# Kernel tuning notes

Measured on AMD Instinct MI355X. Metric: run time of the kernel, lower is better.

The kernel has to match this reference:

```python
import jax, jax.numpy as jnp
import numpy as np

EMBED_DIM = 64  # scale factor dim (matches head dim)


def setup_inputs() -> dict:
    key0 = jax.random.key(0)
    kq, kk, kv = jax.random.split(key0, 3)
    shape = (2, 16, 2048, 64)  # [B, H, S, D]
    return {
        "query": jax.random.normal(kq, shape, dtype=jnp.float32),
        "key": jax.random.normal(kk, shape, dtype=jnp.float32),
        "value": jax.random.normal(kv, shape, dtype=jnp.float32),
    }


def reference(query, key, value):
    # qk = Q K^T / sqrt(embed_dim); softmax over last dim; @ V
    inv_scale = jnp.sqrt(jnp.asarray(EMBED_DIM, dtype=query.dtype))
    scores = jnp.einsum("bhqd,bhkd->bhqk", query, key) / inv_scale
    probs = jax.nn.softmax(scores, axis=-1)
    # dropout_p=0.0 -> identity (eval semantics)
    return jnp.einsum("bhqk,bhkd->bhqd", probs, value)
```

## Files before the change

### kernel.cpp

```cpp
#include <hip/hip_runtime.h>
#include <hip/hip_bf16.h>

#define S_LEN 2048
#define DDIM  64
#define NT    (S_LEN / 64)
#define SCALE  0.125f
#define SCALE2 0.18033688f
#define NELEM  4194304
#define NQROW  65536

typedef __attribute__((ext_vector_type(8))) short short8;
typedef __attribute__((ext_vector_type(4))) short short4v;
typedef __attribute__((ext_vector_type(4))) float floatx4;

__device__ __forceinline__ short f2bf(float f) {
    union { float f; unsigned u; } v; v.f = f;
    return (short)((v.u + 0x7fffu + ((v.u >> 16) & 1u)) >> 16);
}

__device__ __forceinline__ unsigned pk2bf(float a, float b) {
#if __has_builtin(__builtin_amdgcn_cvt_pk_bf16_f32)
    auto r = __builtin_amdgcn_cvt_pk_bf16_f32(a, b);
    union { decltype(r) v; unsigned u; } c; c.v = r; return c.u;
#else
    union { float f; unsigned u; } x, y; x.f = a; y.f = b;
    unsigned lo = (x.u + 0x7fffu + ((x.u >> 16) & 1u)) >> 16;
    unsigned hi = (y.u + 0x7fffu + ((y.u >> 16) & 1u)) & 0xffff0000u;
    return lo | hi;
#endif
}

__device__ __forceinline__ float fexp2(float x) {
#if __has_builtin(__builtin_amdgcn_exp2f)
    return __builtin_amdgcn_exp2f(x);
#else
    return exp2f(x);
#endif
}

__device__ __forceinline__ void dma16(const void* g, void* l) {
    __builtin_amdgcn_global_load_lds(
        (const __attribute__((address_space(1))) void*)g,
        (__attribute__((address_space(3))) void*)l, 16, 0, 0);
}

__global__ __launch_bounds__(256) void prep_kv(const float* __restrict__ K,
                                               const float* __restrict__ V,
                                               short* __restrict__ Kb,
                                               short* __restrict__ Vt) {
    __shared__ short T[64 * 68];
    const int bh = blockIdx.x & 31;
    const int st = blockIdx.x >> 5;
    const int t  = threadIdx.x;
    const size_t tile_off = (size_t)bh * (S_LEN * DDIM) + (size_t)st * (64 * DDIM);

    {
        const float* src = K + tile_off + t * 16;
        short* dst = Kb + tile_off + t * 16;
        #pragma unroll
        for (int h = 0; h < 2; ++h) {
            float4 a = *(const float4*)(src + h * 8);
            float4 b = *(const float4*)(src + h * 8 + 4);
            uint4 o;
            o.x = pk2bf(a.x, a.y); o.y = pk2bf(a.z, a.w);
            o.z = pk2bf(b.x, b.y); o.w = pk2bf(b.z, b.w);
            *(uint4*)(dst + h * 8) = o;
        }
    }

    const float* src = V + tile_off;
    const int skey = t >> 2, scol = (t & 3) * 4;
    #pragma unroll
    for (int i = 0; i < 4; ++i) {
        const int c = scol + i * 16;
        float4 v = *(const float4*)(src + (size_t)skey * 64 + c);
        uint2 o; o.x = pk2bf(v.x, v.y); o.y = pk2bf(v.z, v.w);
        *(uint2*)&T[skey * 68 + c] = o;
    }
    __syncthreads();
    const int d = t >> 2, cb = (t & 3) * 16;
    short8 o0, o1;
    #pragma unroll
    for (int j = 0; j < 8; ++j) {
        o0[j] = T[(cb + j) * 68 + d];
        o1[j] = T[(cb + 8 + j) * 68 + d];
    }
    short* dst = Vt + (size_t)bh * (DDIM * S_LEN) + (size_t)d * S_LEN + st * 64 + cb;
    *(short8*)dst       = o0;
    *(short8*)(dst + 8) = o1;
}

template <int NSPLIT>
__global__ __launch_bounds__(256) void attn_sm(
    const float* __restrict__ Q, const short* __restrict__ Kb,
    const short* __restrict__ Vt, float* __restrict__ O,
    float* __restrict__ numer, float* __restrict__ denom)
{
    __shared__ short Ks[2][64 * 64];
    __shared__ short Vs[64 * 64];
    __shared__ short Pl[4][32 * 64];

    constexpr int NIT = NT / NSPLIT;

    const int tid  = threadIdx.x;
    const int wave = tid >> 6;
    const int lane = tid & 63;
    const int l16  = lane & 15;
    const int quad = lane >> 4;
    const int x7   = l16 & 7;

    const int bh = blockIdx.x & 31;
    const int rest = blockIdx.x >> 5;
    const int qt = rest & 15;
    const int ks = rest >> 4;
    const size_t base = (size_t)bh * (S_LEN * DDIM);

    const int ci0 = tid,        r0 = ci0 >> 3, c0 = (ci0 & 7) ^ (r0 & 7);
    const int ci1 = 256 + tid,  r1 = ci1 >> 3, c1 = (ci1 & 7) ^ (r1 & 7);
    const size_t koff = (size_t)ks * NIT * (64 * 64);
    const size_t voff = (size_t)ks * NIT * 64;
    const short* pK0 = Kb + base + koff + r0 * 64 + c0 * 8;
    const short* pK1 = Kb + base + koff + r1 * 64 + c1 * 8;
    const short* pV0 = Vt + base + voff + (size_t)r0 * S_LEN + c0 * 8;
    const short* pV1 = Vt + base + voff + (size_t)r1 * S_LEN + c1 * 8;

    dma16(pK0, &Ks[0][ci0 * 8]);
    dma16(pK1, &Ks[0][ci1 * 8]);

    short8 qf[2][2];
    #pragma unroll
    for (int nq = 0; nq < 2; ++nq) {
        const float* qp = Q + base + (size_t)(qt * 128 + wave * 32 + nq * 16 + l16) * 64 + quad * 8;
        #pragma unroll
        for (int kt = 0; kt < 2; ++kt) {
            float4 a = *(const float4*)(qp + kt * 32);
            float4 b = *(const float4*)(qp + kt * 32 + 4);
            union { unsigned u[4]; short8 s; } qc;
            qc.u[0] = pk2bf(a.x * SCALE2, a.y * SCALE2);
            qc.u[1] = pk2bf(a.z * SCALE2, a.w * SCALE2);
            qc.u[2] = pk2bf(b.x * SCALE2, b.y * SCALE2);
            qc.u[3] = pk2bf(b.z * SCALE2, b.w * SCALE2);
            qf[nq][kt] = qc.s;
        }
    }

    floatx4 oacc[2][4];
    float rs[2];
    #pragma unroll
    for (int mt = 0; mt < 2; ++mt) {
        #pragma unroll
        for (int dt = 0; dt < 4; ++dt) oacc[mt][dt] = (floatx4){0.f,0.f,0.f,0.f};
        rs[mt] = 0.f;
    }

    short* Pw = &Pl[wave][0];

    for (int kb = 0; kb < NIT; ++kb) {
        const int cur = kb & 1;
        __syncthreads();

        {
            const int ov = kb * 64;
            dma16(pV0 + ov, &Vs[ci0 * 8]);
            dma16(pV1 + ov, &Vs[ci1 * 8]);
        }
        if (kb + 1 < NIT) {
            const int ok = (kb + 1) * (64 * 64);
            dma16(pK0 + ok, &Ks[cur ^ 1][ci0 * 8]);
            dma16(pK1 + ok, &Ks[cur ^ 1][ci1 * 8]);
        }

        const short* ks_ = Ks[cur];
        floatx4 sc[2][4];
        #pragma unroll
        for (int mk = 0; mk < 4; ++mk) {
            floatx4 a0 = (floatx4){0.f,0.f,0.f,0.f};
            floatx4 a1 = (floatx4){0.f,0.f,0.f,0.f};
            #pragma unroll
            for (int kt = 0; kt < 2; ++kt) {
                const int csw = (kt * 4 + quad) ^ x7;
                short8 kf = *(const short8*)&ks_[(mk * 16 + l16) * 64 + csw * 8];
                a0 = __builtin_amdgcn_mfma_f32_16x16x32_bf16(kf, qf[0][kt], a0, 0, 0, 0);
                a1 = __builtin_amdgcn_mfma_f32_16x16x32_bf16(kf, qf[1][kt], a1, 0, 0, 0);
            }
            sc[0][mk] = a0; sc[1][mk] = a1;
        }

        #pragma unroll
        for (int nq = 0; nq < 2; ++nq) {
            const int prow = (nq * 16 + l16) * 64;
            #pragma unroll
            for (int mk = 0; mk < 4; ++mk) {
                float p0 = fexp2(sc[nq][mk][0]);
                float p1 = fexp2(sc[nq][mk][1]);
                float p2 = fexp2(sc[nq][mk][2]);
                float p3 = fexp2(sc[nq][mk][3]);
                rs[nq] += (p0 + p1) + (p2 + p3);
                uint2 pv; pv.x = pk2bf(p0, p1); pv.y = pk2bf(p2, p3);
                const int c8 = (mk * 4 + quad) ^ (2 * x7);
                *(uint2*)&Pw[prow + c8 * 4] = pv;
            }
        }

        __syncthreads();

        #pragma unroll
        for (int kt = 0; kt < 2; ++kt) {
            const int csw = (kt * 4 + quad) ^ x7;
            short8 pf0 = *(const short8*)&Pw[(l16)      * 64 + csw * 8];
            short8 pf1 = *(const short8*)&Pw[(16 + l16) * 64 + csw * 8];
            #pragma unroll
            for (int dt = 0; dt < 4; ++dt) {
                short8 vf = *(const short8*)&Vs[(dt * 16 + l16) * 64 + csw * 8];
                oacc[0][dt] = __builtin_amdgcn_mfma_f32_16x16x32_bf16(pf0, vf, oacc[0][dt], 0, 0, 0);
                oacc[1][dt] = __builtin_amdgcn_mfma_f32_16x16x32_bf16(pf1, vf, oacc[1][dt], 0, 0, 0);
            }
        }
    }

    float inv[2];
    #pragma unroll
    for (int nq = 0; nq < 2; ++nq) {
        float s = rs[nq];
        s += __shfl_xor(s, 16, 64);
        s += __shfl_xor(s, 32, 64);
        if (NSPLIT == 2) {
            if (quad == 0)
                denom[(size_t)ks * NQROW + bh * S_LEN + qt * 128 + wave * 32 + nq * 16 + l16] = s;
        }
        inv[nq] = 1.0f / s;
    }

    #pragma unroll
    for (int mt = 0; mt < 2; ++mt) {
        #pragma unroll
        for (int r = 0; r < 4; ++r) {
            const int row = qt * 128 + wave * 32 + mt * 16 + quad * 4 + r;
            if (NSPLIT == 1) {
                const float d_r = __shfl(inv[mt], quad * 4 + r, 64);
                float* op = O + base + (size_t)row * 64 + l16;
                #pragma unroll
                for (int dt = 0; dt < 4; ++dt)
                    op[dt * 16] = oacc[mt][dt][r] * d_r;
            } else {
                float* np = numer + (size_t)ks * NELEM + base + (size_t)row * 64 + l16;
                #pragma unroll
                for (int dt = 0; dt < 4; ++dt)
                    np[dt * 16] = oacc[mt][dt][r];
            }
        }
    }
}

__global__ __launch_bounds__(256) void combine2(const float* __restrict__ numer,
                                                const float* __restrict__ denom,
                                                float* __restrict__ O) {
    const size_t i = ((size_t)blockIdx.x * 256 + threadIdx.x) * 4;
    const size_t q = i >> 6;
    const float inv = 1.0f / (denom[q] + denom[NQROW + q]);
    float4 n0 = *(const float4*)(numer + i);
    float4 n1 = *(const float4*)(numer + NELEM + i);
    float4 o;
    o.x = (n0.x + n1.x) * inv;
    o.y = (n0.y + n1.y) * inv;
    o.z = (n0.z + n1.z) * inv;
    o.w = (n0.w + n1.w) * inv;
    *(float4*)(O + i) = o;
}

#define BQ    64
#define BKEY  64
#define KPAD  72

__global__ __launch_bounds__(256) void attn_kernel(
    const float* __restrict__ Q, const float* __restrict__ K,
    const float* __restrict__ V, float* __restrict__ O)
{
    __shared__ short Ksh[BKEY * KPAD];
    __shared__ short Vtt[DDIM * KPAD];
    __shared__ short Pls[4][16 * KPAD];

    const int tid  = threadIdx.x;
    const int wave = tid >> 6;
    const int lane = tid & 63;
    const int l16  = lane & 15;
    const int quad = lane >> 4;

    const int bh = blockIdx.x & 31;
    const int qt = blockIdx.x >> 5;
    const size_t base = (size_t)bh * S_LEN * DDIM;

    const int qrow = qt * BQ + wave * 16 + l16;
    short8 qf[2];
    {
        const float* qp = Q + base + (size_t)qrow * DDIM + quad * 8;
        #pragma unroll
        for (int kt = 0; kt < 2; ++kt) {
            float4 a = *(const float4*)(qp + kt * 32);
            float4 b = *(const float4*)(qp + kt * 32 + 4);
            short* d = (short*)&qf[kt];
            d[0]=f2bf(a.x*SCALE); d[1]=f2bf(a.y*SCALE); d[2]=f2bf(a.z*SCALE); d[3]=f2bf(a.w*SCALE);
            d[4]=f2bf(b.x*SCALE); d[5]=f2bf(b.y*SCALE); d[6]=f2bf(b.z*SCALE); d[7]=f2bf(b.w*SCALE);
        }
    }

    float m_i[4], l_i[4];
    floatx4 oacc[4];
    #pragma unroll
    for (int r = 0; r < 4; ++r) { m_i[r] = -3.0e38f; l_i[r] = 0.f; }
    #pragma unroll
    for (int dt = 0; dt < 4; ++dt) oacc[dt] = (floatx4){0.f, 0.f, 0.f, 0.f};

    const int skey = tid >> 2;
    const int scol = (tid & 3) * 4;

    for (int kb = 0; kb < S_LEN / BKEY; ++kb) {
        const float* Kg = K + base + (size_t)kb * BKEY * DDIM + (size_t)skey * DDIM;
        const float* Vg = V + base + (size_t)kb * BKEY * DDIM + (size_t)skey * DDIM;
        #pragma unroll
        for (int i = 0; i < 4; ++i) {
            const int c = scol + i * 16;
            float4 kv = *(const float4*)(Kg + c);
            short* kd = &Ksh[skey * KPAD + c];
            kd[0]=f2bf(kv.x); kd[1]=f2bf(kv.y); kd[2]=f2bf(kv.z); kd[3]=f2bf(kv.w);
            float4 vv = *(const float4*)(Vg + c);
            Vtt[(c+0)*KPAD + skey] = f2bf(vv.x);
            Vtt[(c+1)*KPAD + skey] = f2bf(vv.y);
            Vtt[(c+2)*KPAD + skey] = f2bf(vv.z);
            Vtt[(c+3)*KPAD + skey] = f2bf(vv.w);
        }
        __syncthreads();

        floatx4 sc[4];
        #pragma unroll
        for (int nt = 0; nt < 4; ++nt) {
            floatx4 acc = (floatx4){0.f, 0.f, 0.f, 0.f};
            #pragma unroll
            for (int kt = 0; kt < 2; ++kt) {
                short8 kf = *(const short8*)&Ksh[(nt*16 + l16) * KPAD + kt*32 + quad*8];
                acc = __builtin_amdgcn_mfma_f32_16x16x32_bf16(qf[kt], kf, acc, 0, 0, 0);
            }
            sc[nt] = acc;
        }

        short* Pw = &Pls[wave][0];
        #pragma unroll
        for (int r = 0; r < 4; ++r) {
            float mx = fmaxf(fmaxf(sc[0][r], sc[1][r]), fmaxf(sc[2][r], sc[3][r]));
            #pragma unroll
            for (int off = 1; off < 16; off <<= 1)
                mx = fmaxf(mx, __shfl_xor(mx, off, 64));
            const float mnew  = fmaxf(m_i[r], mx);
            const float alpha = __expf(m_i[r] - mnew);
            m_i[r] = mnew;
            float rsum = 0.f;
            #pragma unroll
            for (int nt = 0; nt < 4; ++nt) {
                float p = __expf(sc[nt][r] - mnew);
                rsum += p;
                Pw[(quad*4 + r) * KPAD + nt*16 + l16] = f2bf(p);
            }
            #pragma unroll
            for (int off = 1; off < 16; off <<= 1)
                rsum += __shfl_xor(rsum, off, 64);
            l_i[r] = l_i[r] * alpha + rsum;
            oacc[0][r] *= alpha; oacc[1][r] *= alpha;
            oacc[2][r] *= alpha; oacc[3][r] *= alpha;
        }

        #pragma unroll
        for (int kt = 0; kt < 2; ++kt) {
            short8 pf = *(const short8*)&Pw[l16 * KPAD + kt*32 + quad*8];
            #pragma unroll
            for (int dt = 0; dt < 4; ++dt) {
                short8 vf = *(const short8*)&Vtt[(dt*16 + l16) * KPAD + kt*32 + quad*8];
                oacc[dt] = __builtin_amdgcn_mfma_f32_16x16x32_bf16(pf, vf, oacc[dt], 0, 0, 0);
            }
        }
        __syncthreads();
    }

    #pragma unroll
    for (int r = 0; r < 4; ++r) {
        const float inv = 1.0f / l_i[r];
        const int row = qt * BQ + wave * 16 + quad * 4 + r;
        float* op = O + base + (size_t)row * DDIM + l16;
        #pragma unroll
        for (int dt = 0; dt < 4; ++dt)
            op[dt * 16] = oacc[dt][r] * inv;
    }
}

extern "C" void kernel_launch(void* const* d_in, const int* in_sizes, int n_in,
                              void* d_out, int out_size, void* d_ws, size_t ws_size,
                              hipStream_t stream) {
    const float* Q = (const float*)d_in[0];
    const float* K = (const float*)d_in[1];
    const float* V = (const float*)d_in[2];
    float* O = (float*)d_out;

    const size_t prep_bytes = (size_t)NELEM * 2 * 2;
    const size_t split_bytes = prep_bytes + (size_t)2 * NELEM * 4
                             + (size_t)2 * NQROW * 4;

    if (ws_size >= split_bytes) {
        short* Kb  = (short*)d_ws;
        short* Vtp = (short*)d_ws + NELEM;
        float* num = (float*)((char*)d_ws + prep_bytes);
        float* den = num + (size_t)2 * NELEM;
        prep_kv<<<dim3(1024), dim3(256), 0, stream>>>(K, V, Kb, Vtp);
        attn_sm<2><<<dim3(1024), dim3(256), 0, stream>>>(Q, Kb, Vtp, nullptr, num, den);
        combine2<<<dim3(NELEM / 1024), dim3(256), 0, stream>>>(num, den, O);
    } else if (ws_size >= prep_bytes) {
        short* Kb  = (short*)d_ws;
        short* Vtp = (short*)d_ws + NELEM;
        prep_kv<<<dim3(1024), dim3(256), 0, stream>>>(K, V, Kb, Vtp);
        attn_sm<1><<<dim3(512), dim3(256), 0, stream>>>(Q, Kb, Vtp, O, nullptr, nullptr);
    } else {
        attn_kernel<<<dim3(1024), dim3(256), 0, stream>>>(Q, K, V, O);
    }
}
```

Before: 160.9 us.

## Prefetch K/V tiles through registers and transpose V without LDS

The attention loop no longer issues direct global-to-LDS DMA with a double-buffered K tile. It now loads the next K and V tiles into registers one iteration ahead, stores them to a single LDS buffer, and syncs with an explicit lgkm waitcnt plus barrier. The second per-iteration __syncthreads after the P write is removed, since each wave's P buffer is private. The prep kernel now transposes V in registers with a 4x4 per-thread gather instead of going through shared memory. The aim is fewer barriers and less LDS work, at the cost of extra VGPRs for the prefetched tiles and a single-buffered K tile.

```diff
diff --git a/kernel.cpp b/kernel.cpp
--- a/kernel.cpp
+++ b/kernel.cpp
@@ -8,6 +8,7 @@
 #define SCALE2 0.18033688f
 #define NELEM  4194304
 #define NQROW  65536
+#define WC_LGKM0 0xc07f
 
 typedef __attribute__((ext_vector_type(8))) short short8;
 typedef __attribute__((ext_vector_type(4))) short short4v;
@@ -38,17 +39,10 @@
 #endif
 }
 
-__device__ __forceinline__ void dma16(const void* g, void* l) {
-    __builtin_amdgcn_global_load_lds(
-        (const __attribute__((address_space(1))) void*)g,
-        (__attribute__((address_space(3))) void*)l, 16, 0, 0);
-}
-
 __global__ __launch_bounds__(256) void prep_kv(const float* __restrict__ K,
                                                const float* __restrict__ V,
                                                short* __restrict__ Kb,
                                                short* __restrict__ Vt) {
-    __shared__ short T[64 * 68];
     const int bh = blockIdx.x & 31;
     const int st = blockIdx.x >> 5;
     const int t  = threadIdx.x;
@@ -68,26 +62,27 @@
         }
     }
 
-    const float* src = V + tile_off;
-    const int skey = t >> 2, scol = (t & 3) * 4;
-    #pragma unroll
-    for (int i = 0; i < 4; ++i) {
-        const int c = scol + i * 16;
-        float4 v = *(const float4*)(src + (size_t)skey * 64 + c);
-        uint2 o; o.x = pk2bf(v.x, v.y); o.y = pk2bf(v.z, v.w);
-        *(uint2*)&T[skey * 68 + c] = o;
-    }
-    __syncthreads();
-    const int d = t >> 2, cb = (t & 3) * 16;
-    short8 o0, o1;
-    #pragma unroll
-    for (int j = 0; j < 8; ++j) {
-        o0[j] = T[(cb + j) * 68 + d];
-        o1[j] = T[(cb + 8 + j) * 68 + d];
-    }
-    short* dst = Vt + (size_t)bh * (DDIM * S_LEN) + (size_t)d * S_LEN + st * 64 + cb;
-    *(short8*)dst       = o0;
-    *(short8*)(dst + 8) = o1;
+    {
+        const int s4 = (t & 15) * 4;
+        const int d4 = (t >> 4) * 4;
+        const float* src = V + tile_off;
+        float4 v0 = *(const float4*)(src + (size_t)(s4 + 0) * 64 + d4);
+        float4 v1 = *(const float4*)(src + (size_t)(s4 + 1) * 64 + d4);
+        float4 v2 = *(const float4*)(src + (size_t)(s4 + 2) * 64 + d4);
+        float4 v3 = *(const float4*)(src + (size_t)(s4 + 3) * 64 + d4);
+        const float* r0 = (const float*)&v0;
+        const float* r1 = (const float*)&v1;
+        const float* r2 = (const float*)&v2;
+        const float* r3 = (const float*)&v3;
+        short* dstb = Vt + (size_t)bh * (DDIM * S_LEN) + (size_t)st * 64 + s4;
+        #pragma unroll
+        for (int dd = 0; dd < 4; ++dd) {
+            uint2 o;
+            o.x = pk2bf(r0[dd], r1[dd]);
+            o.y = pk2bf(r2[dd], r3[dd]);
+            *(uint2*)(dstb + (size_t)(d4 + dd) * S_LEN) = o;
+        }
+    }
 }
 
 template <int NSPLIT>
@@ -96,7 +91,7 @@
     const short* __restrict__ Vt, float* __restrict__ O,
     float* __restrict__ numer, float* __restrict__ denom)
 {
-    __shared__ short Ks[2][64 * 64];
+    __shared__ short Ks[64 * 64];
     __shared__ short Vs[64 * 64];
     __shared__ short Pl[4][32 * 64];
 
@@ -124,8 +119,10 @@
     const short* pV0 = Vt + base + voff + (size_t)r0 * S_LEN + c0 * 8;
     const short* pV1 = Vt + base + voff + (size_t)r1 * S_LEN + c1 * 8;
 
-    dma16(pK0, &Ks[0][ci0 * 8]);
-    dma16(pK1, &Ks[0][ci1 * 8]);
+    short8 rk0 = *(const short8*)pK0;
+    short8 rk1 = *(const short8*)pK1;
+    short8 rv0 = *(const short8*)pV0;
+    short8 rv1 = *(const short8*)pV1;
 
     short8 qf[2][2];
     #pragma unroll
@@ -156,21 +153,24 @@
     short* Pw = &Pl[wave][0];
 
     for (int kb = 0; kb < NIT; ++kb) {
-        const int cur = kb & 1;
-        __syncthreads();
-
-        {
-            const int ov = kb * 64;
-            dma16(pV0 + ov, &Vs[ci0 * 8]);
-            dma16(pV1 + ov, &Vs[ci1 * 8]);
-        }
+        if (kb) __builtin_amdgcn_s_barrier();
+
+        *(short8*)&Ks[ci0 * 8] = rk0;
+        *(short8*)&Ks[ci1 * 8] = rk1;
+        *(short8*)&Vs[ci0 * 8] = rv0;
+        *(short8*)&Vs[ci1 * 8] = rv1;
+
         if (kb + 1 < NIT) {
-            const int ok = (kb + 1) * (64 * 64);
-            dma16(pK0 + ok, &Ks[cur ^ 1][ci0 * 8]);
-            dma16(pK1 + ok, &Ks[cur ^ 1][ci1 * 8]);
-        }
-
-        const short* ks_ = Ks[cur];
+            const int ok = (kb + 1) * (64 * 64), ov = (kb + 1) * 64;
+            rk0 = *(const short8*)(pK0 + ok);
+            rk1 = *(const short8*)(pK1 + ok);
+            rv0 = *(const short8*)(pV0 + ov);
+            rv1 = *(const short8*)(pV1 + ov);
+        }
+
+        __builtin_amdgcn_s_waitcnt(WC_LGKM0);
+        __builtin_amdgcn_s_barrier();
+
         floatx4 sc[2][4];
         #pragma unroll
         for (int mk = 0; mk < 4; ++mk) {
@@ -179,7 +179,7 @@
             #pragma unroll
             for (int kt = 0; kt < 2; ++kt) {
                 const int csw = (kt * 4 + quad) ^ x7;
-                short8 kf = *(const short8*)&ks_[(mk * 16 + l16) * 64 + csw * 8];
+                short8 kf = *(const short8*)&Ks[(mk * 16 + l16) * 64 + csw * 8];
                 a0 = __builtin_amdgcn_mfma_f32_16x16x32_bf16(kf, qf[0][kt], a0, 0, 0, 0);
                 a1 = __builtin_amdgcn_mfma_f32_16x16x32_bf16(kf, qf[1][kt], a1, 0, 0, 0);
             }
@@ -201,8 +201,6 @@
                 *(uint2*)&Pw[prow + c8 * 4] = pv;
             }
         }
-
-        __syncthreads();
 
         #pragma unroll
         for (int kt = 0; kt < 2; ++kt) {
```

Result: faster. 152.2 us (-5.4%).
